# Kernel tuning notes

Measured on AMD Instinct MI355X. Metric: run time of the kernel, lower is better.

## Reference

```python
import jax, jax.numpy as jnp
import numpy as np
import math

N, E, D = 50000, 800000, 128


def _linear_params(key, d_in, d_out):
    kw, kb = jax.random.split(key)
    s = 1.0 / math.sqrt(d_in)
    W = jax.random.uniform(kw, (d_out, d_in), minval=-s, maxval=s, dtype=jnp.float32)
    b = jax.random.uniform(kb, (d_out,), minval=-s, maxval=s, dtype=jnp.float32)
    return W, b


def setup_inputs() -> dict:
    key = jax.random.key(0)
    ks = jax.random.split(key, 10)
    inp = {
        "x": jax.random.normal(ks[0], (N, D), dtype=jnp.float32),
        "edge_index": jax.random.randint(ks[1], (2, E), 0, N, dtype=jnp.int32),
    }
    # BPPGraphEncoder: two attention layers, each with q/k/v linears (D->D)
    names = ["q1", "k1", "v1", "q2", "k2", "v2"]
    for i, nm in enumerate(names):
        W, b = _linear_params(ks[2 + i], D, D)
        inp[f"W{nm}"], inp[f"b{nm}"] = W, b
    # SecondaryStructureEncoder: two linears (D->D)
    inp["Ws1"], inp["bs1"] = _linear_params(ks[8], D, D)
    inp["Ws2"], inp["bs2"] = _linear_params(ks[9], D, D)
    return inp


def _attention_layer(x, row, col, Wq, bq, Wk, bk, Wv, bv):
    Q = x @ Wq.T + bq          # [N, D]
    K = x @ Wk.T + bk
    V = x @ Wv.T + bv
    # per-edge score, softmax over ALL edges (faithful to F.softmax(scores, dim=0))
    scores = jnp.sum(Q[row] * K[col], axis=-1) / math.sqrt(Q.shape[-1])  # [E]
    alpha = jax.nn.softmax(scores)                                       # [E]
    msg = alpha[:, None] * V[col]                                        # [E, D]
    return jax.ops.segment_sum(msg, row, num_segments=x.shape[0])        # [N, D]


def _ss_layer(x, row, col, W, b, deg):
    agg = jax.ops.segment_sum(x[col], row, num_segments=x.shape[0])
    return jax.nn.relu((agg / deg) @ W.T + b)


def reference(x, edge_index, Wq1, bq1, Wk1, bk1, Wv1, bv1,
              Wq2, bq2, Wk2, bk2, Wv2, bv2, Ws1, bs1, Ws2, bs2):
    row, col = edge_index[0], edge_index[1]
    # BPPGraphEncoder.forward
    h = jax.nn.elu(_attention_layer(x, row, col, Wq1, bq1, Wk1, bk1, Wv1, bv1))
    bpp_out = _attention_layer(h, row, col, Wq2, bq2, Wk2, bk2, Wv2, bv2)
    # SecondaryStructureEncoder.forward (degree-normalized message passing)
    deg = jax.ops.segment_sum(jnp.ones((row.shape[0],), jnp.float32), row,
                              num_segments=x.shape[0])
    deg = jnp.clip(deg, 1.0, None)[:, None]                              # [N, 1]
    s = _ss_layer(x, row, col, Ws1, bs1, deg)
    ss_out = _ss_layer(s, row, col, Ws2, bs2, deg)
    return jnp.concatenate([bpp_out, ss_out], axis=-1)                   # [N, 2D]
```

## Files before the change

kernel.cpp:

```cpp
#include <hip/hip_runtime.h>
#include <math.h>

#define FD 128

typedef __attribute__((ext_vector_type(8))) _Float16 half8v;
typedef __attribute__((ext_vector_type(4))) _Float16 half4v;
typedef __attribute__((ext_vector_type(4))) float float4v;
typedef __attribute__((ext_vector_type(2))) float floatx2;

static __device__ __forceinline__ void dec8(unsigned int lo, unsigned int hi, float* f){
  floatx2 a = __builtin_amdgcn_cvt_pk_f32_fp8(lo, false);
  floatx2 b = __builtin_amdgcn_cvt_pk_f32_fp8(lo, true);
  floatx2 c = __builtin_amdgcn_cvt_pk_f32_fp8(hi, false);
  floatx2 d = __builtin_amdgcn_cvt_pk_f32_fp8(hi, true);
  f[0]=a[0]; f[1]=a[1]; f[2]=b[0]; f[3]=b[1];
  f[4]=c[0]; f[5]=c[1]; f[6]=d[0]; f[7]=d[1];
}

__global__ void k_cvt_x(const float4* __restrict__ in, half4v* __restrict__ out, int n4){
  int i = blockIdx.x * 256 + threadIdx.x, st = gridDim.x * 256;
  for (; i < n4; i += st){
    float4 v = in[i];
    half4v o;
    o[0] = (_Float16)v.x; o[1] = (_Float16)v.y; o[2] = (_Float16)v.z; o[3] = (_Float16)v.w;
    out[i] = o;
  }
}

__global__ __launch_bounds__(256) void k_cvt_w(
    const float* __restrict__ w0, const float* __restrict__ w1, const float* __restrict__ w2,
    const float* __restrict__ w3, const float* __restrict__ w4, const float* __restrict__ w5,
    const float* __restrict__ w6, const float* __restrict__ w7, _Float16* __restrict__ dst){
  int i = blockIdx.x * 256 + threadIdx.x;
  if (i >= FD * FD) return;
  dst[0*FD*FD + i] = (_Float16)w0[i];
  dst[1*FD*FD + i] = (_Float16)w1[i];
  dst[2*FD*FD + i] = (_Float16)w2[i];
  dst[3*FD*FD + i] = (_Float16)w3[i];
  dst[4*FD*FD + i] = (_Float16)w4[i];
  dst[5*FD*FD + i] = (_Float16)w5[i];
  dst[6*FD*FD + i] = (_Float16)w6[i];
  dst[7*FD*FD + i] = (_Float16)w7[i];
}


__global__ __launch_bounds__(256) void k_bhist(const int* __restrict__ row, int E,
    int* __restrict__ bhist){
  __shared__ int h[256];
  h[threadIdx.x] = 0; __syncthreads();
  for (int i = blockIdx.x*256 + threadIdx.x; i < E; i += gridDim.x*256)
    atomicAdd(&h[row[i] >> 8], 1);
  __syncthreads();
  int v = h[threadIdx.x];
  if (v) atomicAdd(&bhist[threadIdx.x], v);
}

__global__ __launch_bounds__(256) void k_bscan(const int* __restrict__ bhist,
    int* __restrict__ bstart, int* __restrict__ bcursor, int E){
  __shared__ int sm[256];
  const int tid = threadIdx.x;
  int v = bhist[tid];
  sm[tid] = v; __syncthreads();
  for (int off = 1; off < 256; off <<= 1){
    int t = (tid >= off) ? sm[tid-off] : 0;
    __syncthreads();
    sm[tid] += t;
    __syncthreads();
  }
  bstart[tid] = sm[tid] - v;
  if (tid == 255) bstart[256] = E;
  bcursor[tid] = 0;
}

__global__ __launch_bounds__(256) void k_bscatter(const int* __restrict__ row,
    const int* __restrict__ col, int E, const int* __restrict__ bstart,
    int* __restrict__ bcursor, uint2* __restrict__ pairs){
  __shared__ int cnt[256];
  __shared__ int base[256];
  const int tid = threadIdx.x;
  const int per = (E + gridDim.x - 1) / gridDim.x;
  const int lo = blockIdx.x * per;
  const int hi = min(E, lo + per);
  cnt[tid] = 0; __syncthreads();
  for (int i = lo + tid; i < hi; i += 256)
    atomicAdd(&cnt[row[i] >> 8], 1);
  __syncthreads();
  base[tid] = cnt[tid] ? atomicAdd(&bcursor[tid], cnt[tid]) : 0;
  __syncthreads();
  cnt[tid] = 0; __syncthreads();
  for (int i = lo + tid; i < hi; i += 256){
    const int r = row[i];
    const int b = r >> 8;
    const int loc = atomicAdd(&cnt[b], 1);
    pairs[(size_t)bstart[b] + base[b] + loc] = make_uint2((unsigned)r, (unsigned)col[i]);
  }
}

__global__ __launch_bounds__(256) void k_bdeg(const uint2* __restrict__ pairs,
    const int* __restrict__ bstart, int N, int* __restrict__ deg){
  __shared__ int cnt[256];
  const int b = blockIdx.x, tid = threadIdx.x;
  cnt[tid] = 0; __syncthreads();
  const int lo = bstart[b], hi = bstart[b+1];
  for (int i = lo + tid; i < hi; i += 256)
    atomicAdd(&cnt[pairs[i].x & 255], 1);
  __syncthreads();
  const int r = (b << 8) + tid;
  if (r < N) deg[r] = cnt[tid];
}

__global__ __launch_bounds__(256) void k_bfill(const uint2* __restrict__ pairs,
    const int* __restrict__ bstart, const int* __restrict__ rowstart, int N,
    int* __restrict__ csrcol){
  __shared__ int base[256];
  __shared__ int cur[256];
  const int b = blockIdx.x, tid = threadIdx.x;
  const int r = (b << 8) + tid;
  base[tid] = (r < N) ? rowstart[r] : 0;
  cur[tid] = 0;
  __syncthreads();
  const int lo = bstart[b], hi = bstart[b+1];
  for (int i = lo + tid; i < hi; i += 256){
    uint2 p = pairs[i];
    const int rl = p.x & 255;
    const int loc = atomicAdd(&cur[rl], 1);
    csrcol[base[rl] + loc] = (int)p.y;
  }
}

__global__ __launch_bounds__(256) void k_scan_blk(const int* __restrict__ in, int n,
    int* __restrict__ out, int* __restrict__ blksum){
  __shared__ int sm[256];
  const int tid = threadIdx.x;
  const int base = blockIdx.x * 1024;
  const int idx = base + tid * 4;
  int v0=0,v1=0,v2=0,v3=0;
  if (idx + 3 < n){ int4 t = *(const int4*)(in + idx); v0=t.x; v1=t.y; v2=t.z; v3=t.w; }
  else {
    if (idx   < n) v0 = in[idx];
    if (idx+1 < n) v1 = in[idx+1];
    if (idx+2 < n) v2 = in[idx+2];
    if (idx+3 < n) v3 = in[idx+3];
  }
  int s = v0+v1+v2+v3;
  sm[tid] = s; __syncthreads();
  for (int off = 1; off < 256; off <<= 1){
    int t = (tid >= off) ? sm[tid-off] : 0;
    __syncthreads();
    sm[tid] += t;
    __syncthreads();
  }
  int excl = sm[tid] - s;
  if (tid == 255) blksum[blockIdx.x] = sm[255];
  if (idx   < n) out[idx]   = excl;
  if (idx+1 < n) out[idx+1] = excl + v0;
  if (idx+2 < n) out[idx+2] = excl + v0 + v1;
  if (idx+3 < n) out[idx+3] = excl + v0 + v1 + v2;
}

__global__ __launch_bounds__(256) void k_scan_part(const int* __restrict__ blksum, int nblk,
    int* __restrict__ blkoff){
  __shared__ int sm[256];
  const int tid = threadIdx.x;
  int v = (tid < nblk) ? blksum[tid] : 0;
  sm[tid] = v; __syncthreads();
  for (int off = 1; off < 256; off <<= 1){
    int t = (tid >= off) ? sm[tid-off] : 0;
    __syncthreads();
    sm[tid] += t;
    __syncthreads();
  }
  if (tid < nblk) blkoff[tid] = sm[tid] - v;
}

__global__ __launch_bounds__(256) void k_scan_add(int* __restrict__ out, int n,
    const int* __restrict__ blkoff, int E){
  int i = blockIdx.x * 256 + threadIdx.x;
  if (i < n) out[i] += blkoff[i >> 10];
  if (i == 0) out[n] = E;
}

template<int NOUT, int ACT, int OMODE>
__global__ __launch_bounds__(256) void k_gemm_lds(const _Float16* __restrict__ X, int ldx,
    const _Float16* __restrict__ W,
    const float* __restrict__ b0, void* __restrict__ Y0,
    const float* __restrict__ b1, void* __restrict__ Y1,
    const float* __restrict__ b2, void* __restrict__ Y2,
    int ldy, int nrows)
{
  __shared__ _Float16 sW[FD * FD];
  const int tid  = threadIdx.x;
  const int wid  = tid >> 6;
  const int lane = tid & 63;
  const int l4 = lane & 15;
  const int kg = lane >> 4;
  const int r0 = blockIdx.x * 64 + wid * 16;

  int rA = r0 + l4; if (rA > nrows - 1) rA = nrows - 1;
  half8v xf[4];
  #pragma unroll
  for (int ks = 0; ks < 4; ks++)
    xf[ks] = *(const half8v*)(X + (size_t)rA * ldx + ks*32 + kg*8);

  for (int o = 0; o < NOUT; o++){
    if (o) __syncthreads();
    const _Float16* Wo = W + (size_t)o * FD * FD;
    #pragma unroll
    for (int j = 0; j < 8; j++){
      const int b = j*4096 + tid*16;
      const int row = b >> 8, cb = b & 255;
      half8v v = *(const half8v*)((const char*)Wo + b);
      *(half8v*)((char*)sW + ((row*256 + (cb ^ ((row & 7) << 4))))) = v;
    }
    __syncthreads();

    float4v acc[8];
    #pragma unroll
    for (int t = 0; t < 8; t++)
      #pragma unroll
      for (int i = 0; i < 4; i++) acc[t][i] = 0.f;

    #pragma unroll
    for (int t = 0; t < 8; t++){
      const int row = t*16 + l4;
      const int sw = (row & 7) << 4;
      #pragma unroll
      for (int ks = 0; ks < 4; ks++){
        half8v wf = *(const half8v*)((const char*)sW + (row*256 + ((ks*64 + kg*16) ^ sw)));
        acc[t] = __builtin_amdgcn_mfma_f32_16x16x32_f16(wf, xf[ks], acc[t], 0, 0, 0);
      }
    }

    const float* bo = (o == 0) ? b0 : (o == 1) ? b1 : b2;
    void* Yo = (o == 0) ? Y0 : (o == 1) ? Y1 : Y2;
    const int r = r0 + l4;
    if (r < nrows){
      #pragma unroll
      for (int t = 0; t < 8; t++){
        const int c = t*16 + kg*4;
        const float4 bb = *(const float4*)(bo + c);
        float v0 = acc[t][0] + bb.x, v1 = acc[t][1] + bb.y;
        float v2 = acc[t][2] + bb.z, v3 = acc[t][3] + bb.w;
        if (ACT){ v0=fmaxf(v0,0.f); v1=fmaxf(v1,0.f); v2=fmaxf(v2,0.f); v3=fmaxf(v3,0.f); }
        if (OMODE == 1 && o == 0){
          *(float4*)((float*)Yo + (size_t)r * ldy + c) = make_float4(v0, v1, v2, v3);
        } else if (OMODE == 2 && o > 0){
          unsigned int w01 = (unsigned int)__builtin_amdgcn_cvt_pk_fp8_f32(v0, v1, 0, false);
          unsigned int w   = (unsigned int)__builtin_amdgcn_cvt_pk_fp8_f32(v2, v3, (int)w01, true);
          *(unsigned int*)((unsigned char*)Yo + (size_t)r * FD + c) = w;
        } else {
          half4v hv;
          hv[0]=(_Float16)v0; hv[1]=(_Float16)v1; hv[2]=(_Float16)v2; hv[3]=(_Float16)v3;
          *(half4v*)((_Float16*)Yo + (size_t)r * ldy + c) = hv;
        }
      }
    }
  }
}

#define SC 0.08838834764831845f

#define RED16(d) \
  d += __shfl_xor(d, 1); d += __shfl_xor(d, 2); d += __shfl_xor(d, 4); d += __shfl_xor(d, 8);

__global__ __launch_bounds__(256) void k_passA(const _Float16* __restrict__ Qh,
    const unsigned char* __restrict__ K8, const _Float16* __restrict__ Xh,
    const int* __restrict__ rowstart, const int* __restrict__ csrcol,
    float* __restrict__ scores, _Float16* __restrict__ SMh, int ldsm, int nnodes)
{
  const int tid = threadIdx.x;
  const int n = blockIdx.x * 16 + (tid >> 4);
  if (n >= nnodes) return;
  const int l4 = tid & 15;
  const half8v qv = *(const half8v*)(Qh + (size_t)n * FD + 8*l4);
  float qf[8];
  #pragma unroll
  for (int i = 0; i < 8; i++) qf[i] = (float)qv[i];
  float sx[8];
  #pragma unroll
  for (int i = 0; i < 8; i++) sx[i] = 0.f;
  const int p0 = rowstart[n], p1 = rowstart[n+1];
  const int last = p1 - 1;
  for (int p = p0; p < p1; p += 4){
    int cc[4]; float mk[4];
    #pragma unroll
    for (int j = 0; j < 4; j++){
      const int idx = p + j;
      cc[j] = csrcol[idx < p1 ? idx : last];
      mk[j] = idx < p1 ? 1.f : 0.f;
    }
    uint2 ku[4]; half8v xv[4];
    #pragma unroll
    for (int j = 0; j < 4; j++){
      ku[j] = *(const uint2*)(K8 + (size_t)cc[j]*FD + 8*l4);
      xv[j] = *(const half8v*)(Xh + (size_t)cc[j]*FD + 8*l4);
    }
    float d[4];
    #pragma unroll
    for (int j = 0; j < 4; j++){
      float kf[8];
      dec8(ku[j].x, ku[j].y, kf);
      float t = 0.f;
      #pragma unroll
      for (int i = 0; i < 8; i++) t += qf[i] * kf[i];
      d[j] = t;
      #pragma unroll
      for (int i = 0; i < 8; i++) sx[i] += mk[j] * (float)xv[j][i];
    }
    #pragma unroll
    for (int j = 0; j < 4; j++){ RED16(d[j]) }
    const float sv = (l4==0) ? d[0] : (l4==1) ? d[1] : (l4==2) ? d[2] : d[3];
    if (l4 < 4 && p + l4 < p1) scores[p + l4] = sv * SC;
  }
  int dg = p1 - p0; if (dg < 1) dg = 1;
  const float inv = 1.f / (float)dg;
  half8v o;
  #pragma unroll
  for (int i = 0; i < 8; i++) o[i] = (_Float16)(sx[i]*inv);
  *(half8v*)(SMh + (size_t)n * ldsm + 8*l4) = o;
}

__global__ __launch_bounds__(256) void k_scores2(const _Float16* __restrict__ Qh,
    const unsigned char* __restrict__ K8,
    const int* __restrict__ rowstart, const int* __restrict__ csrcol,
    float* __restrict__ scores, int nnodes)
{
  const int tid = threadIdx.x;
  const int n = blockIdx.x * 16 + (tid >> 4);
  if (n >= nnodes) return;
  const int l4 = tid & 15;
  const int p0 = rowstart[n], p1 = rowstart[n+1];
  if (p0 >= p1) return;
  const half8v qv = *(const half8v*)(Qh + (size_t)n * FD + 8*l4);
  float qf[8];
  #pragma unroll
  for (int i = 0; i < 8; i++) qf[i] = (float)qv[i];
  const int last = p1 - 1;
  for (int p = p0; p < p1; p += 4){
    int cc[4];
    #pragma unroll
    for (int j = 0; j < 4; j++){
      const int idx = p + j;
      cc[j] = csrcol[idx < p1 ? idx : last];
    }
    uint2 ku[4];
    #pragma unroll
    for (int j = 0; j < 4; j++)
      ku[j] = *(const uint2*)(K8 + (size_t)cc[j]*FD + 8*l4);
    float d[4];
    #pragma unroll
    for (int j = 0; j < 4; j++){
      float kf[8];
      dec8(ku[j].x, ku[j].y, kf);
      float t = 0.f;
      #pragma unroll
      for (int i = 0; i < 8; i++) t += qf[i] * kf[i];
      d[j] = t;
    }
    #pragma unroll
    for (int j = 0; j < 4; j++){ RED16(d[j]) }
    const float sv = (l4==0) ? d[0] : (l4==1) ? d[1] : (l4==2) ? d[2] : d[3];
    if (l4 < 4 && p + l4 < p1) scores[p + l4] = sv * SC;
  }
}

__global__ __launch_bounds__(256) void k_passB(const unsigned char* __restrict__ V8,
    const _Float16* __restrict__ Sh,
    const float* __restrict__ sc, const float* __restrict__ Mp, const float* __restrict__ Ip,
    const int* __restrict__ rowstart, const int* __restrict__ csrcol,
    _Float16* __restrict__ Ah, _Float16* __restrict__ Bh, int ldb, int nnodes)
{
  const int tid = threadIdx.x;
  const int n = blockIdx.x * 16 + (tid >> 4);
  if (n >= nnodes) return;
  const int l4 = tid & 15;
  const float M = Mp[0], inv = Ip[0];
  float av[8], sv[8];
  #pragma unroll
  for (int i = 0; i < 8; i++){ av[i] = 0.f; sv[i] = 0.f; }
  const int p0 = rowstart[n], p1 = rowstart[n+1];
  const int last = p1 - 1;
  for (int p = p0; p < p1; p += 4){
    int cc[4]; float aa[4], mk[4];
    #pragma unroll
    for (int j = 0; j < 4; j++){
      const int idx = p + j;
      const int eff = idx < p1 ? idx : last;
      cc[j] = csrcol[eff];
      aa[j] = sc[eff];
      mk[j] = idx < p1 ? 1.f : 0.f;
    }
    uint2 vu[4]; half8v ss[4];
    #pragma unroll
    for (int j = 0; j < 4; j++){
      vu[j] = *(const uint2*)(V8 + (size_t)cc[j]*FD + 8*l4);
      ss[j] = *(const half8v*)(Sh + (size_t)cc[j]*FD + 8*l4);
    }
    #pragma unroll
    for (int j = 0; j < 4; j++){
      const float a = mk[j] * __expf(aa[j] - M);
      float vf[8];
      dec8(vu[j].x, vu[j].y, vf);
      #pragma unroll
      for (int i = 0; i < 8; i++){
        av[i] += a * vf[i];
        sv[i] += mk[j] * (float)ss[j][i];
      }
    }
  }
  #pragma unroll
  for (int i = 0; i < 8; i++){
    float v = av[i] * inv;
    av[i] = v > 0.f ? v : expm1f(v);
  }
  half8v oa;
  #pragma unroll
  for (int i = 0; i < 8; i++) oa[i] = (_Float16)av[i];
  *(half8v*)(Ah + (size_t)n * FD + 8*l4) = oa;
  int dg = p1 - p0; if (dg < 1) dg = 1;
  const float invd = 1.f / (float)dg;
  half8v ob;
  #pragma unroll
  for (int i = 0; i < 8; i++) ob[i] = (_Float16)(sv[i]*invd);
  *(half8v*)(Bh + (size_t)n * ldb + 8*l4) = ob;
}

__global__ __launch_bounds__(256) void k_message2(const unsigned char* __restrict__ V8,
    const float* __restrict__ sc, const float* __restrict__ Mp, const float* __restrict__ Ip,
    const int* __restrict__ rowstart, const int* __restrict__ csrcol,
    float* __restrict__ out, int ldo, int nnodes)
{
  const int tid = threadIdx.x;
  const int n = blockIdx.x * 16 + (tid >> 4);
  if (n >= nnodes) return;
  const int l4 = tid & 15;
  const float M = Mp[0], inv = Ip[0];
  float av[8];
  #pragma unroll
  for (int i = 0; i < 8; i++) av[i] = 0.f;
  const int p0 = rowstart[n], p1 = rowstart[n+1];
  const int last = p1 - 1;
  for (int p = p0; p < p1; p += 4){
    int cc[4]; float aa[4], mk[4];
    #pragma unroll
    for (int j = 0; j < 4; j++){
      const int idx = p + j;
      const int eff = idx < p1 ? idx : last;
      cc[j] = csrcol[eff];
      aa[j] = sc[eff];
      mk[j] = idx < p1 ? 1.f : 0.f;
    }
    uint2 vu[4];
    #pragma unroll
    for (int j = 0; j < 4; j++)
      vu[j] = *(const uint2*)(V8 + (size_t)cc[j]*FD + 8*l4);
    #pragma unroll
    for (int j = 0; j < 4; j++){
      const float a = mk[j] * __expf(aa[j] - M);
      float vf[8];
      dec8(vu[j].x, vu[j].y, vf);
      #pragma unroll
      for (int i = 0; i < 8; i++) av[i] += a * vf[i];
    }
  }
  float* op = out + (size_t)n * ldo + 8*l4;
  *(float4*)(op    ) = make_float4(av[0]*inv, av[1]*inv, av[2]*inv, av[3]*inv);
  *(float4*)(op + 4) = make_float4(av[4]*inv, av[5]*inv, av[6]*inv, av[7]*inv);
}

__global__ __launch_bounds__(256) void k_sm_partial(const float* __restrict__ s, int n,
    float* __restrict__ pm, float* __restrict__ ps){
  __shared__ float sm_m[256], sm_s[256];
  const int tid = threadIdx.x;
  float m = -3.402823466e38f, sum = 0.f;
  const int n4 = n >> 2;
  const float4* s4 = (const float4*)s;
  for (int i = blockIdx.x * 256 + tid; i < n4; i += gridDim.x * 256){
    float4 q = s4[i];
    float vv[4] = {q.x, q.y, q.z, q.w};
    #pragma unroll
    for (int j = 0; j < 4; j++){
      float v = vv[j];
      if (v <= m) sum += __expf(v - m);
      else { sum = sum * __expf(m - v) + 1.f; m = v; }
    }
  }
  if (blockIdx.x == 0 && tid < (n - (n4 << 2))){
    float v = s[(n4 << 2) + tid];
    if (v <= m) sum += __expf(v - m);
    else { sum = sum * __expf(m - v) + 1.f; m = v; }
  }
  sm_m[tid] = m; sm_s[tid] = sum; __syncthreads();
  for (int off = 128; off > 0; off >>= 1){
    if (tid < off){
      float m2 = sm_m[tid + off], s2 = sm_s[tid + off];
      float m1 = sm_m[tid], s1 = sm_s[tid];
      float Mx = fmaxf(m1, m2);
      sm_m[tid] = Mx;
      sm_s[tid] = s1 * __expf(m1 - Mx) + s2 * __expf(m2 - Mx);
    }
    __syncthreads();
  }
  if (tid == 0){ pm[blockIdx.x] = sm_m[0]; ps[blockIdx.x] = sm_s[0]; }
}

__global__ __launch_bounds__(256) void k_sm_final(const float* __restrict__ pm, const float* __restrict__ ps,
    int n, float* __restrict__ Mout, float* __restrict__ Iout){
  __shared__ float sm_m[256], sm_s[256];
  const int tid = threadIdx.x;
  float m = -3.402823466e38f, sum = 0.f;
  for (int i = tid; i < n; i += 256){
    float m2 = pm[i], s2 = ps[i];
    float Mx = fmaxf(m, m2);
    sum = sum * __expf(m - Mx) + s2 * __expf(m2 - Mx);
    m = Mx;
  }
  sm_m[tid] = m; sm_s[tid] = sum; __syncthreads();
  for (int off = 128; off > 0; off >>= 1){
    if (tid < off){
      float m2 = sm_m[tid + off], s2 = sm_s[tid + off];
      float m1 = sm_m[tid], s1 = sm_s[tid];
      float Mx = fmaxf(m1, m2);
      sm_m[tid] = Mx;
      sm_s[tid] = s1 * __expf(m1 - Mx) + s2 * __expf(m2 - Mx);
    }
    __syncthreads();
  }
  if (tid == 0){ Mout[0] = sm_m[0]; Iout[0] = 1.f / sm_s[0]; }
}

extern "C" void kernel_launch(void* const* d_in, const int* in_sizes, int n_in,
                              void* d_out, int out_size, void* d_ws, size_t ws_size,
                              hipStream_t stream)
{
  const float* x   = (const float*)d_in[0];
  const int*   ei  = (const int*)d_in[1];
  const float* Wq1 = (const float*)d_in[2];  const float* bq1 = (const float*)d_in[3];
  const float* Wk1 = (const float*)d_in[4];  const float* bk1 = (const float*)d_in[5];
  const float* Wv1 = (const float*)d_in[6];  const float* bv1 = (const float*)d_in[7];
  const float* Wq2 = (const float*)d_in[8];  const float* bq2 = (const float*)d_in[9];
  const float* Wk2 = (const float*)d_in[10]; const float* bk2 = (const float*)d_in[11];
  const float* Wv2 = (const float*)d_in[12]; const float* bv2 = (const float*)d_in[13];
  const float* Ws1 = (const float*)d_in[14]; const float* bs1 = (const float*)d_in[15];
  const float* Ws2 = (const float*)d_in[16]; const float* bs2 = (const float*)d_in[17];

  const int N = in_sizes[0] / FD;
  const int E = in_sizes[1] / 2;
  const int* row = ei;
  const int* col = ei + E;
  float* out = (float*)d_out;

  char* ws = (char*)d_ws;
  size_t off = 0;
  auto alloc = [&](size_t bytes) -> void* {
    void* p = ws + off;
    off += (bytes + 255) & ~(size_t)255;
    return p;
  };
  int* deg      = (int*)alloc((size_t)N * 4);
  int* rowstart = (int*)alloc((size_t)(N + 1) * 4);
  int* csrcol   = (int*)alloc((size_t)E * 4);
  uint2* pairs  = (uint2*)alloc((size_t)E * 8);
  int* bhist    = (int*)alloc(1024);
  int* bstart   = (int*)alloc(1056);
  int* bcursor  = (int*)alloc(1024);
  float* scores = (float*)alloc((size_t)E * 4);
  int* blksum   = (int*)alloc(1024);
  int* blkoff   = (int*)alloc(1024);
  float* pm     = (float*)alloc(1024);
  float* ps     = (float*)alloc(1024);
  float* Mv     = (float*)alloc(256);
  float* Iv     = (float*)alloc(256);
  _Float16* Xh = (_Float16*)alloc((size_t)N * FD * 2);
  _Float16* Qh = (_Float16*)alloc((size_t)N * FD * 2);
  unsigned char* K8 = (unsigned char*)alloc((size_t)N * FD);
  unsigned char* V8 = (unsigned char*)alloc((size_t)N * FD);
  _Float16* Ah = (_Float16*)alloc((size_t)N * FD * 2);
  _Float16* Wh = (_Float16*)alloc((size_t)8 * FD * FD * 2);
  _Float16* Sh = Xh;
  _Float16* SMBh = (_Float16*)out;
  (void)ws_size; (void)n_in; (void)out_size;

  hipMemsetAsync(bhist, 0, 1024, stream);

  k_cvt_x<<<2048, 256, 0, stream>>>((const float4*)x, (half4v*)Xh, N * FD / 4);
  k_cvt_w<<<(FD*FD + 255)/256, 256, 0, stream>>>(Wq1, Wk1, Wv1, Wq2, Wk2, Wv2, Ws1, Ws2, Wh);

  const int nbuckets = (N + 255) >> 8;
  const int nblk = (N + 1023) / 1024;
  k_bhist<<<1024, 256, 0, stream>>>(row, E, bhist);
  k_bscan<<<1, 256, 0, stream>>>(bhist, bstart, bcursor, E);
  k_bscatter<<<256, 256, 0, stream>>>(row, col, E, bstart, bcursor, pairs);
  k_bdeg<<<nbuckets, 256, 0, stream>>>(pairs, bstart, N, deg);
  k_scan_blk<<<nblk, 256, 0, stream>>>(deg, N, rowstart, blksum);
  k_scan_part<<<1, 256, 0, stream>>>(blksum, nblk, blkoff);
  k_scan_add<<<(N + 255)/256, 256, 0, stream>>>(rowstart, N, blkoff, E);
  k_bfill<<<nbuckets, 256, 0, stream>>>(pairs, bstart, rowstart, N, csrcol);

  const int gb = (N + 63) / 64;
  const int nb = (N + 15) / 16;
  const int rb = 256;

  k_gemm_lds<3,0,2><<<gb, 256, 0, stream>>>(Xh, FD, Wh + 0*FD*FD,
      bq1, Qh, bk1, K8, bv1, V8, FD, N);

  k_passA<<<nb, 256, 0, stream>>>(Qh, K8, Xh, rowstart, csrcol, scores, SMBh, 512, N);

  k_sm_partial<<<rb, 256, 0, stream>>>(scores, E, pm, ps);
  k_sm_final<<<1, 256, 0, stream>>>(pm, ps, rb, Mv, Iv);

  k_gemm_lds<1,1,0><<<gb, 256, 0, stream>>>(SMBh, 512, Wh + 6*FD*FD,
      bs1, Sh, nullptr, nullptr, nullptr, nullptr, FD, N);

  k_passB<<<nb, 256, 0, stream>>>(V8, Sh, scores, Mv, Iv, rowstart, csrcol, Ah, SMBh, 512, N);

  k_gemm_lds<1,1,1><<<gb, 256, 0, stream>>>(SMBh, 512, Wh + 7*FD*FD,
      bs2, out + FD, nullptr, nullptr, nullptr, nullptr, 2*FD, N);

  k_gemm_lds<3,0,2><<<gb, 256, 0, stream>>>(Ah, FD, Wh + 3*FD*FD,
      bq2, Qh, bk2, K8, bv2, V8, FD, N);
  k_scores2<<<nb, 256, 0, stream>>>(Qh, K8, rowstart, csrcol, scores, N);

  k_sm_partial<<<rb, 256, 0, stream>>>(scores, E, pm, ps);
  k_sm_final<<<1, 256, 0, stream>>>(pm, ps, rb, Mv, Iv);

  k_message2<<<nb, 256, 0, stream>>>(V8, scores, Mv, Iv, rowstart, csrcol, out, 2*FD, N);
}
```

Measured before the change: 298.6 us.

## Fuse online-softmax partial reduction into score kernels and merge conversion kernels

Score kernels now keep a per-thread online max/sum of the scores they write and reduce it per block into pm/ps, so the separate k_sm_partial pass that re-read all E scores is gone. k_sm_final now reduces over nb (about 3125) block partials instead of 256. The x and weight fp32-to-fp16 conversions are merged into one launch. In exchange, the block-level reduction and its syncthreads run inside the gather kernels, and the single-block final reduction has more partials to process.

```diff
diff --git a/kernel.cpp b/kernel.cpp
--- a/kernel.cpp
+++ b/kernel.cpp
@@ -17,32 +17,34 @@
   f[4]=c[0]; f[5]=c[1]; f[6]=d[0]; f[7]=d[1];
 }
 
-__global__ void k_cvt_x(const float4* __restrict__ in, half4v* __restrict__ out, int n4){
-  int i = blockIdx.x * 256 + threadIdx.x, st = gridDim.x * 256;
-  for (; i < n4; i += st){
-    float4 v = in[i];
-    half4v o;
-    o[0] = (_Float16)v.x; o[1] = (_Float16)v.y; o[2] = (_Float16)v.z; o[3] = (_Float16)v.w;
-    out[i] = o;
-  }
-}
-
-__global__ __launch_bounds__(256) void k_cvt_w(
+#define OSM_PUSH(om, os, v) \
+  { if ((v) <= om) os += __expf((v) - om); \
+    else { os = os * __expf(om - (v)) + 1.f; om = (v); } }
+
+__global__ void k_cvt_all(const float4* __restrict__ x4, half4v* __restrict__ Xh4, int n4x,
     const float* __restrict__ w0, const float* __restrict__ w1, const float* __restrict__ w2,
     const float* __restrict__ w3, const float* __restrict__ w4, const float* __restrict__ w5,
-    const float* __restrict__ w6, const float* __restrict__ w7, _Float16* __restrict__ dst){
-  int i = blockIdx.x * 256 + threadIdx.x;
-  if (i >= FD * FD) return;
-  dst[0*FD*FD + i] = (_Float16)w0[i];
-  dst[1*FD*FD + i] = (_Float16)w1[i];
-  dst[2*FD*FD + i] = (_Float16)w2[i];
-  dst[3*FD*FD + i] = (_Float16)w3[i];
-  dst[4*FD*FD + i] = (_Float16)w4[i];
-  dst[5*FD*FD + i] = (_Float16)w5[i];
-  dst[6*FD*FD + i] = (_Float16)w6[i];
-  dst[7*FD*FD + i] = (_Float16)w7[i];
-}
-
+    const float* __restrict__ w6, const float* __restrict__ w7, _Float16* __restrict__ Wh){
+  const int nw4 = 8 * FD * FD / 4;
+  int i = blockIdx.x * 256 + threadIdx.x, st = gridDim.x * 256;
+  for (; i < nw4 + n4x; i += st){
+    if (i < nw4){
+      const int m = i >> 12;
+      const int e = (i & 4095) << 2;
+      const float* wm = (m==0)?w0:(m==1)?w1:(m==2)?w2:(m==3)?w3:(m==4)?w4:(m==5)?w5:(m==6)?w6:w7;
+      float4 v = *(const float4*)(wm + e);
+      half4v o;
+      o[0]=(_Float16)v.x; o[1]=(_Float16)v.y; o[2]=(_Float16)v.z; o[3]=(_Float16)v.w;
+      *(half4v*)(Wh + (size_t)m * FD * FD + e) = o;
+    } else {
+      const int j = i - nw4;
+      float4 v = x4[j];
+      half4v o;
+      o[0]=(_Float16)v.x; o[1]=(_Float16)v.y; o[2]=(_Float16)v.z; o[3]=(_Float16)v.w;
+      Xh4[j] = o;
+    }
+  }
+}
 
 __global__ __launch_bounds__(256) void k_bhist(const int* __restrict__ row, int E,
     int* __restrict__ bhist){
@@ -266,102 +268,144 @@
 __global__ __launch_bounds__(256) void k_passA(const _Float16* __restrict__ Qh,
     const unsigned char* __restrict__ K8, const _Float16* __restrict__ Xh,
     const int* __restrict__ rowstart, const int* __restrict__ csrcol,
-    float* __restrict__ scores, _Float16* __restrict__ SMh, int ldsm, int nnodes)
+    float* __restrict__ scores, _Float16* __restrict__ SMh, int ldsm,
+    float* __restrict__ pm, float* __restrict__ ps, int nnodes)
 {
+  __shared__ float red_m[256], red_s[256];
   const int tid = threadIdx.x;
   const int n = blockIdx.x * 16 + (tid >> 4);
-  if (n >= nnodes) return;
   const int l4 = tid & 15;
-  const half8v qv = *(const half8v*)(Qh + (size_t)n * FD + 8*l4);
-  float qf[8];
-  #pragma unroll
-  for (int i = 0; i < 8; i++) qf[i] = (float)qv[i];
-  float sx[8];
-  #pragma unroll
-  for (int i = 0; i < 8; i++) sx[i] = 0.f;
-  const int p0 = rowstart[n], p1 = rowstart[n+1];
-  const int last = p1 - 1;
-  for (int p = p0; p < p1; p += 4){
-    int cc[4]; float mk[4];
-    #pragma unroll
-    for (int j = 0; j < 4; j++){
-      const int idx = p + j;
-      cc[j] = csrcol[idx < p1 ? idx : last];
-      mk[j] = idx < p1 ? 1.f : 0.f;
-    }
-    uint2 ku[4]; half8v xv[4];
-    #pragma unroll
-    for (int j = 0; j < 4; j++){
-      ku[j] = *(const uint2*)(K8 + (size_t)cc[j]*FD + 8*l4);
-      xv[j] = *(const half8v*)(Xh + (size_t)cc[j]*FD + 8*l4);
-    }
-    float d[4];
-    #pragma unroll
-    for (int j = 0; j < 4; j++){
-      float kf[8];
-      dec8(ku[j].x, ku[j].y, kf);
-      float t = 0.f;
-      #pragma unroll
-      for (int i = 0; i < 8; i++) t += qf[i] * kf[i];
-      d[j] = t;
-      #pragma unroll
-      for (int i = 0; i < 8; i++) sx[i] += mk[j] * (float)xv[j][i];
-    }
-    #pragma unroll
-    for (int j = 0; j < 4; j++){ RED16(d[j]) }
-    const float sv = (l4==0) ? d[0] : (l4==1) ? d[1] : (l4==2) ? d[2] : d[3];
-    if (l4 < 4 && p + l4 < p1) scores[p + l4] = sv * SC;
-  }
-  int dg = p1 - p0; if (dg < 1) dg = 1;
-  const float inv = 1.f / (float)dg;
-  half8v o;
-  #pragma unroll
-  for (int i = 0; i < 8; i++) o[i] = (_Float16)(sx[i]*inv);
-  *(half8v*)(SMh + (size_t)n * ldsm + 8*l4) = o;
+  float om = -3.402823466e38f, os = 0.f;
+  if (n < nnodes){
+    const half8v qv = *(const half8v*)(Qh + (size_t)n * FD + 8*l4);
+    float qf[8];
+    #pragma unroll
+    for (int i = 0; i < 8; i++) qf[i] = (float)qv[i];
+    float sx[8];
+    #pragma unroll
+    for (int i = 0; i < 8; i++) sx[i] = 0.f;
+    const int p0 = rowstart[n], p1 = rowstart[n+1];
+    const int last = p1 - 1;
+    for (int p = p0; p < p1; p += 4){
+      int cc[4]; float mk[4];
+      #pragma unroll
+      for (int j = 0; j < 4; j++){
+        const int idx = p + j;
+        cc[j] = csrcol[idx < p1 ? idx : last];
+        mk[j] = idx < p1 ? 1.f : 0.f;
+      }
+      uint2 ku[4]; half8v xv[4];
+      #pragma unroll
+      for (int j = 0; j < 4; j++){
+        ku[j] = *(const uint2*)(K8 + (size_t)cc[j]*FD + 8*l4);
+        xv[j] = *(const half8v*)(Xh + (size_t)cc[j]*FD + 8*l4);
+      }
+      float d[4];
+      #pragma unroll
+      for (int j = 0; j < 4; j++){
+        float kf[8];
+        dec8(ku[j].x, ku[j].y, kf);
+        float t = 0.f;
+        #pragma unroll
+        for (int i = 0; i < 8; i++) t += qf[i] * kf[i];
+        d[j] = t;
+        #pragma unroll
+        for (int i = 0; i < 8; i++) sx[i] += mk[j] * (float)xv[j][i];
+      }
+      #pragma unroll
+      for (int j = 0; j < 4; j++){ RED16(d[j]) }
+      const float sv = (l4==0) ? d[0] : (l4==1) ? d[1] : (l4==2) ? d[2] : d[3];
+      if (l4 < 4 && p + l4 < p1){
+        const float scv = sv * SC;
+        scores[p + l4] = scv;
+        OSM_PUSH(om, os, scv)
+      }
+    }
+    int dg = p1 - p0; if (dg < 1) dg = 1;
+    const float inv = 1.f / (float)dg;
+    half8v o;
+    #pragma unroll
+    for (int i = 0; i < 8; i++) o[i] = (_Float16)(sx[i]*inv);
+    *(half8v*)(SMh + (size_t)n * ldsm + 8*l4) = o;
+  }
+  red_m[tid] = om; red_s[tid] = os;
+  __syncthreads();
+  for (int off = 128; off > 0; off >>= 1){
+    if (tid < off){
+      float m2 = red_m[tid + off], s2 = red_s[tid + off];
+      float m1 = red_m[tid], s1 = red_s[tid];
+      float Mx = fmaxf(m1, m2);
+      red_m[tid] = Mx;
+      red_s[tid] = s1 * __expf(m1 - Mx) + s2 * __expf(m2 - Mx);
+    }
+    __syncthreads();
+  }
+  if (tid == 0){ pm[blockIdx.x] = red_m[0]; ps[blockIdx.x] = red_s[0]; }
 }
 
 __global__ __launch_bounds__(256) void k_scores2(const _Float16* __restrict__ Qh,
     const unsigned char* __restrict__ K8,
     const int* __restrict__ rowstart, const int* __restrict__ csrcol,
-    float* __restrict__ scores, int nnodes)
+    float* __restrict__ scores, float* __restrict__ pm, float* __restrict__ ps, int nnodes)
 {
+  __shared__ float red_m[256], red_s[256];
   const int tid = threadIdx.x;
   const int n = blockIdx.x * 16 + (tid >> 4);
-  if (n >= nnodes) return;
   const int l4 = tid & 15;
-  const int p0 = rowstart[n], p1 = rowstart[n+1];
-  if (p0 >= p1) return;
-  const half8v qv = *(const half8v*)(Qh + (size_t)n * FD + 8*l4);
-  float qf[8];
-  #pragma unroll
-  for (int i = 0; i < 8; i++) qf[i] = (float)qv[i];
-  const int last = p1 - 1;
-  for (int p = p0; p < p1; p += 4){
-    int cc[4];
-    #pragma unroll
-    for (int j = 0; j < 4; j++){
-      const int idx = p + j;
-      cc[j] = csrcol[idx < p1 ? idx : last];
-    }
-    uint2 ku[4];
-    #pragma unroll
-    for (int j = 0; j < 4; j++)
-      ku[j] = *(const uint2*)(K8 + (size_t)cc[j]*FD + 8*l4);
-    float d[4];
-    #pragma unroll
-    for (int j = 0; j < 4; j++){
-      float kf[8];
-      dec8(ku[j].x, ku[j].y, kf);
-      float t = 0.f;
-      #pragma unroll
-      for (int i = 0; i < 8; i++) t += qf[i] * kf[i];
-      d[j] = t;
-    }
-    #pragma unroll
-    for (int j = 0; j < 4; j++){ RED16(d[j]) }
-    const float sv = (l4==0) ? d[0] : (l4==1) ? d[1] : (l4==2) ? d[2] : d[3];
-    if (l4 < 4 && p + l4 < p1) scores[p + l4] = sv * SC;
-  }
+  float om = -3.402823466e38f, os = 0.f;
+  if (n < nnodes){
+    const int p0 = rowstart[n], p1 = rowstart[n+1];
+    if (p0 < p1){
+      const half8v qv = *(const half8v*)(Qh + (size_t)n * FD + 8*l4);
+      float qf[8];
+      #pragma unroll
+      for (int i = 0; i < 8; i++) qf[i] = (float)qv[i];
+      const int last = p1 - 1;
+      for (int p = p0; p < p1; p += 4){
+        int cc[4];
+        #pragma unroll
+        for (int j = 0; j < 4; j++){
+          const int idx = p + j;
+          cc[j] = csrcol[idx < p1 ? idx : last];
+        }
+        uint2 ku[4];
+        #pragma unroll
+        for (int j = 0; j < 4; j++)
+          ku[j] = *(const uint2*)(K8 + (size_t)cc[j]*FD + 8*l4);
+        float d[4];
+        #pragma unroll
+        for (int j = 0; j < 4; j++){
+          float kf[8];
+          dec8(ku[j].x, ku[j].y, kf);
+          float t = 0.f;
+          #pragma unroll
+          for (int i = 0; i < 8; i++) t += qf[i] * kf[i];
+          d[j] = t;
+        }
+        #pragma unroll
+        for (int j = 0; j < 4; j++){ RED16(d[j]) }
+        const float sv = (l4==0) ? d[0] : (l4==1) ? d[1] : (l4==2) ? d[2] : d[3];
+        if (l4 < 4 && p + l4 < p1){
+          const float scv = sv * SC;
+          scores[p + l4] = scv;
+          OSM_PUSH(om, os, scv)
+        }
+      }
+    }
+  }
+  red_m[tid] = om; red_s[tid] = os;
+  __syncthreads();
+  for (int off = 128; off > 0; off >>= 1){
+    if (tid < off){
+      float m2 = red_m[tid + off], s2 = red_s[tid + off];
+      float m1 = red_m[tid], s1 = red_s[tid];
+      float Mx = fmaxf(m1, m2);
+      red_m[tid] = Mx;
+      red_s[tid] = s1 * __expf(m1 - Mx) + s2 * __expf(m2 - Mx);
+    }
+    __syncthreads();
+  }
+  if (tid == 0){ pm[blockIdx.x] = red_m[0]; ps[blockIdx.x] = red_s[0]; }
 }
 
 __global__ __launch_bounds__(256) void k_passB(const unsigned char* __restrict__ V8,
@@ -466,42 +510,6 @@
   float* op = out + (size_t)n * ldo + 8*l4;
   *(float4*)(op    ) = make_float4(av[0]*inv, av[1]*inv, av[2]*inv, av[3]*inv);
   *(float4*)(op + 4) = make_float4(av[4]*inv, av[5]*inv, av[6]*inv, av[7]*inv);
-}
-
-__global__ __launch_bounds__(256) void k_sm_partial(const float* __restrict__ s, int n,
-    float* __restrict__ pm, float* __restrict__ ps){
-  __shared__ float sm_m[256], sm_s[256];
-  const int tid = threadIdx.x;
-  float m = -3.402823466e38f, sum = 0.f;
-  const int n4 = n >> 2;
-  const float4* s4 = (const float4*)s;
-  for (int i = blockIdx.x * 256 + tid; i < n4; i += gridDim.x * 256){
-    float4 q = s4[i];
-    float vv[4] = {q.x, q.y, q.z, q.w};
-    #pragma unroll
-    for (int j = 0; j < 4; j++){
-      float v = vv[j];
-      if (v <= m) sum += __expf(v - m);
-      else { sum = sum * __expf(m - v) + 1.f; m = v; }
-    }
-  }
-  if (blockIdx.x == 0 && tid < (n - (n4 << 2))){
-    float v = s[(n4 << 2) + tid];
-    if (v <= m) sum += __expf(v - m);
-    else { sum = sum * __expf(m - v) + 1.f; m = v; }
-  }
-  sm_m[tid] = m; sm_s[tid] = sum; __syncthreads();
-  for (int off = 128; off > 0; off >>= 1){
-    if (tid < off){
-      float m2 = sm_m[tid + off], s2 = sm_s[tid + off];
-      float m1 = sm_m[tid], s1 = sm_s[tid];
-      float Mx = fmaxf(m1, m2);
-      sm_m[tid] = Mx;
-      sm_s[tid] = s1 * __expf(m1 - Mx) + s2 * __expf(m2 - Mx);
-    }
-    __syncthreads();
-  }
-  if (tid == 0){ pm[blockIdx.x] = sm_m[0]; ps[blockIdx.x] = sm_s[0]; }
 }
 
 __global__ __launch_bounds__(256) void k_sm_final(const float* __restrict__ pm, const float* __restrict__ ps,
@@ -557,6 +565,7 @@
     off += (bytes + 255) & ~(size_t)255;
     return p;
   };
+  const int nb = (N + 15) / 16;
   int* deg      = (int*)alloc((size_t)N * 4);
   int* rowstart = (int*)alloc((size_t)(N + 1) * 4);
   int* csrcol   = (int*)alloc((size_t)E * 4);
@@ -567,8 +576,8 @@
   float* scores = (float*)alloc((size_t)E * 4);
   int* blksum   = (int*)alloc(1024);
   int* blkoff   = (int*)alloc(1024);
-  float* pm     = (float*)alloc(1024);
-  float* ps     = (float*)alloc(1024);
+  float* pm     = (float*)alloc((size_t)nb * 4);
+  float* ps     = (float*)alloc((size_t)nb * 4);
   float* Mv     = (float*)alloc(256);
   float* Iv     = (float*)alloc(256);
   _Float16* Xh = (_Float16*)alloc((size_t)N * FD * 2);
@@ -583,8 +592,8 @@
 
   hipMemsetAsync(bhist, 0, 1024, stream);
 
-  k_cvt_x<<<2048, 256, 0, stream>>>((const float4*)x, (half4v*)Xh, N * FD / 4);
-  k_cvt_w<<<(FD*FD + 255)/256, 256, 0, stream>>>(Wq1, Wk1, Wv1, Wq2, Wk2, Wv2, Ws1, Ws2, Wh);
+  k_cvt_all<<<2048, 256, 0, stream>>>((const float4*)x, (half4v*)Xh, N * FD / 4,
+      Wq1, Wk1, Wv1, Wq2, Wk2, Wv2, Ws1, Ws2, Wh);
 
   const int nbuckets = (N + 255) >> 8;
   const int nblk = (N + 1023) / 1024;
@@ -598,16 +607,12 @@
   k_bfill<<<nbuckets, 256, 0, stream>>>(pairs, bstart, rowstart, N, csrcol);
 
   const int gb = (N + 63) / 64;
-  const int nb = (N + 15) / 16;
-  const int rb = 256;
 
   k_gemm_lds<3,0,2><<<gb, 256, 0, stream>>>(Xh, FD, Wh + 0*FD*FD,
       bq1, Qh, bk1, K8, bv1, V8, FD, N);
 
-  k_passA<<<nb, 256, 0, stream>>>(Qh, K8, Xh, rowstart, csrcol, scores, SMBh, 512, N);
-
-  k_sm_partial<<<rb, 256, 0, stream>>>(scores, E, pm, ps);
-  k_sm_final<<<1, 256, 0, stream>>>(pm, ps, rb, Mv, Iv);
+  k_passA<<<nb, 256, 0, stream>>>(Qh, K8, Xh, rowstart, csrcol, scores, SMBh, 512, pm, ps, N);
+  k_sm_final<<<1, 256, 0, stream>>>(pm, ps, nb, Mv, Iv);
 
   k_gemm_lds<1,1,0><<<gb, 256, 0, stream>>>(SMBh, 512, Wh + 6*FD*FD,
       bs1, Sh, nullptr, nullptr, nullptr, nullptr, FD, N);
@@ -619,10 +624,8 @@
 
   k_gemm_lds<3,0,2><<<gb, 256, 0, stream>>>(Ah, FD, Wh + 3*FD*FD,
       bq2, Qh, bk2, K8, bv2, V8, FD, N);
-  k_scores2<<<nb, 256, 0, stream>>>(Qh, K8, rowstart, csrcol, scores, N);
-
-  k_sm_partial<<<rb, 256, 0, stream>>>(scores, E, pm, ps);
-  k_sm_final<<<1, 256, 0, stream>>>(pm, ps, rb, Mv, Iv);
+  k_scores2<<<nb, 256, 0, stream>>>(Qh, K8, rowstart, csrcol, scores, pm, ps, N);
+  k_sm_final<<<1, 256, 0, stream>>>(pm, ps, nb, Mv, Iv);
 
   k_message2<<<nb, 256, 0, stream>>>(V8, scores, Mv, Iv, rowstart, csrcol, out, 2*FD, N);
 }
```

Result: no change. 301.5 us (+1.0%).
